# Optimization experiments

Hardware: AMD Instinct MI355X
Metric: run time of the kernel (lower is better)

Reference implementation:

```python
import jax, jax.numpy as jnp
import numpy as np

NUM_CLASSES = 80
NUM_ANCHORS = 3
CONF_TH = 0.5
IOU_TH = 0.4
INPUT_H = 416
INPUT_W = 416
# anchors[i] used for scale i (scale1=stride8, scale2=stride16, scale3=stride32)
ANCHORS = np.array([[[10, 13], [16, 30], [33, 23]],
                    [[30, 61], [62, 45], [59, 119]],
                    [[116, 90], [156, 198], [373, 326]]], dtype=np.float32)


def setup_inputs() -> dict:
    key = jax.random.key(0)
    k1, k2, k3 = jax.random.split(key, 3)
    B = 4
    C = NUM_ANCHORS * (5 + NUM_CLASSES)  # 255
    return {
        'scale1': jax.random.normal(k1, (B, C, 52, 52), dtype=jnp.float32),
        'scale2': jax.random.normal(k2, (B, C, 26, 26), dtype=jnp.float32),
        'scale3': jax.random.normal(k3, (B, C, 13, 13), dtype=jnp.float32),
    }


def _decode(feat, anchors_s):
    # feat: [B, 3*(5+nc), H, W]; matches torch transpose(1,3)+reshape ordering
    B, C, H, W = feat.shape
    bbox_size = C // NUM_ANCHORS
    p = jnp.transpose(feat, (0, 3, 2, 1)).reshape(B, W * H * NUM_ANCHORS, bbox_size)
    xy = jax.nn.sigmoid(p[..., :2])
    conf_cls = jax.nn.sigmoid(p[..., 4:])
    # grid offsets: flat index = w*(H*3) + h*3 + a, offset = (w, h)
    ww, hh = jnp.meshgrid(jnp.arange(W), jnp.arange(H), indexing='ij')  # [W,H]
    cxy = jnp.stack([ww, hh], axis=-1).astype(p.dtype)                  # [W,H,2]
    cxy = jnp.broadcast_to(cxy[:, :, None, :], (W, H, NUM_ANCHORS, 2)).reshape(-1, 2)
    xy = xy + cxy                                                        # [B,N,2]
    anch = jnp.tile(anchors_s.astype(p.dtype), (H * W, 1))               # [N,2], anchor fastest
    wh = jnp.exp(p[..., 2:4]) * anch
    sx = float(INPUT_W // W)
    sy = float(INPUT_H // H)
    scale = jnp.array([sx, sy], dtype=p.dtype)
    xy = xy * scale
    wh = wh * scale
    return jnp.concatenate([xy, wh, conf_cls], axis=-1)  # [B,N,5+nc]


def _nms_image(d):
    # d: [N, 5+nc] decoded predictions for one image
    conf = d[:, 4]
    # bbox columns as in the original: [x-w/2, x+w/2, y-h/2, y+h/2]
    b0 = d[:, 0] - d[:, 2] * 0.5
    b1 = d[:, 0] + d[:, 2] * 0.5
    b2 = d[:, 1] - d[:, 3] * 0.5
    b3 = d[:, 1] + d[:, 3] * 0.5
    cls = jnp.argmax(d[:, 5:], axis=1)
    # bbox_iou reads columns as (xmin, ymin, xmax, ymax) = (b0, b1, b2, b3)
    area = jnp.clip(b2 - b0 + 1.0, 0.0) * jnp.clip(b3 - b1 + 1.0, 0.0)  # [N]
    ixmin = jnp.maximum(b0[:, None], b0[None, :])
    iymin = jnp.maximum(b1[:, None], b1[None, :])
    ixmax = jnp.minimum(b2[:, None], b2[None, :])
    iymax = jnp.minimum(b3[:, None], b3[None, :])
    inter = jnp.clip(ixmax - ixmin + 1.0, 0.0) * jnp.clip(iymax - iymin + 1.0, 0.0)
    iou = inter / (area[:, None] + area[None, :] - inter)  # [N,N]
    valid = conf > CONF_TH
    # faithful to the original masks (including comparing against only valid boxes)
    supp = (iou > IOU_TH) & (cls[:, None] == cls[None, :]) & (conf[:, None] < conf[None, :])
    supp = supp & valid[None, :]
    keep = valid & jnp.any(supp, axis=1)
    det = jnp.stack([b0, b1, b2, b3, conf, cls.astype(d.dtype)], axis=1)  # [N,6]
    return det, keep


def reference(scale1, scale2, scale3):
    d1 = _decode(scale1, jnp.asarray(ANCHORS[0]))
    d2 = _decode(scale2, jnp.asarray(ANCHORS[1]))
    d3 = _decode(scale3, jnp.asarray(ANCHORS[2]))
    decoded = jnp.concatenate([d1, d2, d3], axis=1)  # [B, N, 85]
    # sequential over batch to avoid materializing B NxN IoU matrices at once
    det, keep = jax.lax.map(_nms_image, decoded)     # [B,N,6], [B,N] bool
    return det, keep
```

## Files before the change

### kernel.cpp

```cpp
#include <hip/hip_runtime.h>
#include <math.h>

#define NDET 10647
#define NB 4
#define NCLS 80
#define CAP 160

__device__ __forceinline__ float sigmoidf_ref(float x) {
    if (x >= 0.f) {
        return 1.f / (1.f + expf(-x));
    } else {
        float e = expf(x);
        return e / (1.f + e);
    }
}

template <int S>
__device__ __forceinline__ void decode_cell(
    const float* __restrict__ feat, int b, int a, int cell, int off, float sx,
    float anchw, float anchh, float* __restrict__ det, float* __restrict__ keep,
    int* __restrict__ counts, float4* __restrict__ bbox,
    float* __restrict__ bconf, int* __restrict__ bidx)
{
    const int SS = S * S;
    const int h = cell / S;
    const int w = cell - h * S;
    const float* p = feat + ((size_t)(b * 255 + a * 85)) * SS + cell;

    float t0 = p[0 * SS];
    float t1 = p[1 * SS];
    float t2 = p[2 * SS];
    float t3 = p[3 * SS];
    float t4 = p[4 * SS];

    float v[80];
#pragma unroll
    for (int j = 0; j < 80; ++j) v[j] = p[(size_t)(5 + j) * SS];

    float m0 = v[0], m1 = v[20], m2 = v[40], m3 = v[60];
    int i0 = 0, i1 = 20, i2 = 40, i3 = 60;
#pragma unroll
    for (int j = 1; j < 20; ++j) {
        if (v[j]      > m0) { m0 = v[j];      i0 = j; }
        if (v[20 + j] > m1) { m1 = v[20 + j]; i1 = 20 + j; }
        if (v[40 + j] > m2) { m2 = v[40 + j]; i2 = 40 + j; }
        if (v[60 + j] > m3) { m3 = v[60 + j]; i3 = 60 + j; }
    }
    float best = m0; int cls = i0;
    if (m1 > best) { best = m1; cls = i1; }
    if (m2 > best) { best = m2; cls = i2; }
    if (m3 > best) { best = m3; cls = i3; }

    float x  = (sigmoidf_ref(t0) + (float)w) * sx;
    float y  = (sigmoidf_ref(t1) + (float)h) * sx;
    float bw = expf(t2) * anchw * sx;
    float bh = expf(t3) * anchh * sx;
    float conf = sigmoidf_ref(t4);

    float b0 = x - bw * 0.5f;
    float b1 = x + bw * 0.5f;
    float b2 = y - bh * 0.5f;
    float b3 = y + bh * 0.5f;

    const int n = off + (w * S + h) * 3 + a;
    float2* o = reinterpret_cast<float2*>(det + ((size_t)b * NDET + n) * 6);
    o[0] = make_float2(b0, b1);
    o[1] = make_float2(b2, b3);
    o[2] = make_float2(conf, (float)cls);

    if (conf > 0.5f) {
        int bk = b * NCLS + cls;
        int pos = atomicAdd(&counts[bk], 1);
        if (pos < CAP) {
            int slot = bk * CAP + pos;
            bbox[slot]  = make_float4(b0, b1, b2, b3);
            bconf[slot] = conf;
            bidx[slot]  = n;
        }
    } else {
        keep[(size_t)b * NDET + n] = 0.f;
    }
}

__global__ __launch_bounds__(256) void decode_kernel(
    const float* __restrict__ f0, const float* __restrict__ f1,
    const float* __restrict__ f2, float* __restrict__ det,
    float* __restrict__ keep, int* __restrict__ counts,
    float4* __restrict__ bbox, float* __restrict__ bconf, int* __restrict__ bidx)
{
    const int b = blockIdx.z;
    const int a = blockIdx.y;
    const int cx = blockIdx.x;
    const int tid = threadIdx.x;

    if (cx < 11) {
        int cell = cx * 256 + tid;
        if (cell < 52 * 52) {
            const float aw[3] = {10.f, 16.f, 33.f}, ah[3] = {13.f, 30.f, 23.f};
            decode_cell<52>(f0, b, a, cell, 0, 8.f, aw[a], ah[a],
                            det, keep, counts, bbox, bconf, bidx);
        }
    } else if (cx < 14) {
        int cell = (cx - 11) * 256 + tid;
        if (cell < 26 * 26) {
            const float aw[3] = {30.f, 62.f, 59.f}, ah[3] = {61.f, 45.f, 119.f};
            decode_cell<26>(f1, b, a, cell, 8112, 16.f, aw[a], ah[a],
                            det, keep, counts, bbox, bconf, bidx);
        }
    } else {
        int cell = tid;
        if (cell < 13 * 13) {
            const float aw[3] = {116.f, 156.f, 373.f}, ah[3] = {90.f, 198.f, 326.f};
            decode_cell<13>(f2, b, a, cell, 10140, 32.f, aw[a], ah[a],
                            det, keep, counts, bbox, bconf, bidx);
        }
    }
}

__global__ __launch_bounds__(192) void nms_kernel(
    const int* __restrict__ counts, const float4* __restrict__ bbox,
    const float* __restrict__ bconf, const int* __restrict__ bidx,
    float* __restrict__ keep)
{
    const int bk = blockIdx.x;
    const int b = bk / NCLS;
    int cnt = counts[bk];
    if (cnt > CAP) cnt = CAP;

    __shared__ float4 sb[CAP];
    __shared__ float  sc[CAP];
    __shared__ int    si[CAP];
    const int t = threadIdx.x;
    if (t < cnt) {
        sb[t] = bbox[bk * CAP + t];
        sc[t] = bconf[bk * CAP + t];
        si[t] = bidx[bk * CAP + t];
    }
    __syncthreads();
    if (t >= cnt) return;

    float4 me = sb[t];
    float ci = sc[t];
    float ai = fmaxf(me.z - me.x + 1.f, 0.f) * fmaxf(me.w - me.y + 1.f, 0.f);
    float kv = 0.f;
    for (int j = 0; j < cnt; ++j) {
        float cj = sc[j];
        float4 c = sb[j];
        float xmin = fmaxf(me.x, c.x);
        float ymin = fmaxf(me.y, c.y);
        float xmax = fminf(me.z, c.z);
        float ymax = fminf(me.w, c.w);
        float inter = fmaxf(xmax - xmin + 1.f, 0.f) * fmaxf(ymax - ymin + 1.f, 0.f);
        float aj = fmaxf(c.z - c.x + 1.f, 0.f) * fmaxf(c.w - c.y + 1.f, 0.f);
        float iou = inter / (ai + aj - inter);
        if (cj > ci && iou > 0.4f) kv = 1.f;
    }
    keep[(size_t)b * NDET + si[t]] = kv;
}

extern "C" void kernel_launch(void* const* d_in, const int* in_sizes, int n_in,
                              void* d_out, int out_size, void* d_ws, size_t ws_size,
                              hipStream_t stream) {
    const float* f0 = (const float*)d_in[0];
    const float* f1 = (const float*)d_in[1];
    const float* f2 = (const float*)d_in[2];
    float* det  = (float*)d_out;
    float* keep = det + (size_t)NB * NDET * 6;

    char* ws = (char*)d_ws;
    int* counts = (int*)ws;                             ws += NB * NCLS * sizeof(int);
    ws = (char*)(((uintptr_t)ws + 15) & ~(uintptr_t)15);
    float4* bbox = (float4*)ws;                         ws += (size_t)NB * NCLS * CAP * sizeof(float4);
    float* bconf = (float*)ws;                          ws += (size_t)NB * NCLS * CAP * sizeof(float);
    int*   bidx  = (int*)ws;

    hipMemsetAsync(counts, 0, NB * NCLS * sizeof(int), stream);

    dim3 gdec(15, 3, NB);
    hipLaunchKernelGGL(decode_kernel, gdec, dim3(256), 0, stream,
                       f0, f1, f2, det, keep, counts, bbox, bconf, bidx);

    hipLaunchKernelGGL(nms_kernel, dim3(NB * NCLS), dim3(192), 0, stream,
                       counts, bbox, bconf, bidx, keep);
}
```

Measured before the change: 33.84 us.

## Fuse decode and per-class NMS into one cooperative kernel with grid sync

Merges the decode and NMS kernels into a single cooperative launch of 320 blocks. The first 180 blocks decode cells, a grid-wide sync follows, and then each block runs NMS for one (batch, class) bucket. This is meant to remove one kernel launch and the gap between the two kernels. In exchange it adds a grid barrier and the cost of a cooperative launch, and NMS now runs with 256 threads per block instead of 192.

```diff
diff --git a/kernel.cpp b/kernel.cpp
--- a/kernel.cpp
+++ b/kernel.cpp
@@ -1,5 +1,8 @@
 #include <hip/hip_runtime.h>
+#include <hip/hip_cooperative_groups.h>
 #include <math.h>
+
+namespace cg = cooperative_groups;
 
 #define NDET 10647
 #define NB 4
@@ -82,47 +85,48 @@
     }
 }
 
-__global__ __launch_bounds__(256) void decode_kernel(
+__global__ __launch_bounds__(256) void fused_kernel(
     const float* __restrict__ f0, const float* __restrict__ f1,
     const float* __restrict__ f2, float* __restrict__ det,
     float* __restrict__ keep, int* __restrict__ counts,
     float4* __restrict__ bbox, float* __restrict__ bconf, int* __restrict__ bidx)
 {
-    const int b = blockIdx.z;
-    const int a = blockIdx.y;
-    const int cx = blockIdx.x;
+    const int bx = blockIdx.x;
     const int tid = threadIdx.x;
 
-    if (cx < 11) {
-        int cell = cx * 256 + tid;
-        if (cell < 52 * 52) {
-            const float aw[3] = {10.f, 16.f, 33.f}, ah[3] = {13.f, 30.f, 23.f};
-            decode_cell<52>(f0, b, a, cell, 0, 8.f, aw[a], ah[a],
-                            det, keep, counts, bbox, bconf, bidx);
-        }
-    } else if (cx < 14) {
-        int cell = (cx - 11) * 256 + tid;
-        if (cell < 26 * 26) {
-            const float aw[3] = {30.f, 62.f, 59.f}, ah[3] = {61.f, 45.f, 119.f};
-            decode_cell<26>(f1, b, a, cell, 8112, 16.f, aw[a], ah[a],
-                            det, keep, counts, bbox, bconf, bidx);
-        }
-    } else {
-        int cell = tid;
-        if (cell < 13 * 13) {
-            const float aw[3] = {116.f, 156.f, 373.f}, ah[3] = {90.f, 198.f, 326.f};
-            decode_cell<13>(f2, b, a, cell, 10140, 32.f, aw[a], ah[a],
-                            det, keep, counts, bbox, bconf, bidx);
+    if (bx < 180) {
+        const int cx = bx % 15;
+        const int ab = bx / 15;
+        const int a = ab % 3;
+        const int b = ab / 3;
+
+        if (cx < 11) {
+            int cell = cx * 256 + tid;
+            if (cell < 52 * 52) {
+                const float aw[3] = {10.f, 16.f, 33.f}, ah[3] = {13.f, 30.f, 23.f};
+                decode_cell<52>(f0, b, a, cell, 0, 8.f, aw[a], ah[a],
+                                det, keep, counts, bbox, bconf, bidx);
+            }
+        } else if (cx < 14) {
+            int cell = (cx - 11) * 256 + tid;
+            if (cell < 26 * 26) {
+                const float aw[3] = {30.f, 62.f, 59.f}, ah[3] = {61.f, 45.f, 119.f};
+                decode_cell<26>(f1, b, a, cell, 8112, 16.f, aw[a], ah[a],
+                                det, keep, counts, bbox, bconf, bidx);
+            }
+        } else {
+            int cell = tid;
+            if (cell < 13 * 13) {
+                const float aw[3] = {116.f, 156.f, 373.f}, ah[3] = {90.f, 198.f, 326.f};
+                decode_cell<13>(f2, b, a, cell, 10140, 32.f, aw[a], ah[a],
+                                det, keep, counts, bbox, bconf, bidx);
+            }
         }
     }
-}
 
-__global__ __launch_bounds__(192) void nms_kernel(
-    const int* __restrict__ counts, const float4* __restrict__ bbox,
-    const float* __restrict__ bconf, const int* __restrict__ bidx,
-    float* __restrict__ keep)
-{
-    const int bk = blockIdx.x;
+    cg::this_grid().sync();
+
+    const int bk = bx;
     const int b = bk / NCLS;
     int cnt = counts[bk];
     if (cnt > CAP) cnt = CAP;
@@ -130,7 +134,7 @@
     __shared__ float4 sb[CAP];
     __shared__ float  sc[CAP];
     __shared__ int    si[CAP];
-    const int t = threadIdx.x;
+    const int t = tid;
     if (t < cnt) {
         sb[t] = bbox[bk * CAP + t];
         sc[t] = bconf[bk * CAP + t];
@@ -176,10 +180,9 @@
 
     hipMemsetAsync(counts, 0, NB * NCLS * sizeof(int), stream);
 
-    dim3 gdec(15, 3, NB);
-    hipLaunchKernelGGL(decode_kernel, gdec, dim3(256), 0, stream,
-                       f0, f1, f2, det, keep, counts, bbox, bconf, bidx);
-
-    hipLaunchKernelGGL(nms_kernel, dim3(NB * NCLS), dim3(192), 0, stream,
-                       counts, bbox, bconf, bidx, keep);
+    void* args[] = { (void*)&f0, (void*)&f1, (void*)&f2, (void*)&det,
+                     (void*)&keep, (void*)&counts, (void*)&bbox,
+                     (void*)&bconf, (void*)&bidx };
+    hipLaunchCooperativeKernel((const void*)fused_kernel, dim3(320), dim3(256),
+                               args, 0, stream);
 }
```

New measurement: 74.84 us. 121% more time.
